# Optimization experiments

Hardware: AMD Instinct MI355X
Metric: run time of the kernel (lower is better)

## Reference

```python
import jax, jax.numpy as jnp
import numpy as np

R_MAX = 5.0          # MACE default cutoff
P_CUT = 6            # polynomial cutoff exponent
AVG_NEIGH = 16.0     # MACE avg_num_neighbors normalization


def _sph_harm(u):
    """Real spherical harmonics l=0..3, e3nn 'component' normalization. u: [E,3] unit vectors -> [E,16]."""
    x, y, z = u[..., 0], u[..., 1], u[..., 2]
    s3, s5, s15 = np.sqrt(3.0), np.sqrt(5.0), np.sqrt(15.0)
    s35_8, s105, s21_8, s7 = np.sqrt(35.0 / 8.0), np.sqrt(105.0), np.sqrt(21.0 / 8.0), np.sqrt(7.0)
    one = jnp.ones_like(x)
    Y = [
        one,
        s3 * x, s3 * y, s3 * z,
        s15 * x * y, s15 * y * z, 0.5 * s5 * (3.0 * z * z - 1.0), s15 * x * z, 0.5 * s15 * (x * x - y * y),
        s35_8 * y * (3.0 * x * x - y * y), s105 * x * y * z, s21_8 * y * (5.0 * z * z - 1.0),
        0.5 * s7 * (5.0 * z * z * z - 3.0 * z), s21_8 * x * (5.0 * z * z - 1.0),
        0.5 * s105 * z * (x * x - y * y), s35_8 * x * (x * x - 3.0 * y * y),
    ]
    return jnp.stack(Y, axis=-1)


def _radial_embedding(r):
    """Bessel basis (8) times polynomial cutoff. r: [E] -> [E,8]."""
    n = jnp.arange(1, 9, dtype=r.dtype)
    rb = np.sqrt(2.0 / R_MAX) * jnp.sin(n * jnp.pi * r[:, None] / R_MAX) / r[:, None]
    uu = jnp.clip(r / R_MAX, 0.0, 1.0)
    p = float(P_CUT)
    f = (1.0 - 0.5 * (p + 1.0) * (p + 2.0) * uu ** p
         + p * (p + 2.0) * uu ** (p + 1.0)
         - 0.5 * p * (p + 1.0) * uu ** (p + 2.0))
    return rb * f[:, None]


def _forward(positions, shifts, node_attrs, W_embed, W_up, W_r1, W_r2, W_lin, W_skip, W_prod, Wcg, Wcg2, edge_index):
    N = positions.shape[0]
    snd, rcv = edge_index[0], edge_index[1]
    vec = positions[rcv] - positions[snd] + shifts            # [E,3]
    r = jnp.sqrt(jnp.maximum(jnp.sum(vec * vec, -1), 1e-12))  # [E]
    u = vec / r[:, None]
    edge_attrs = _sph_harm(u)                                 # [E,16]
    edge_feats = _radial_embedding(r)                         # [E,8]
    L = edge_attrs.shape[-1]
    k = W_embed.shape[1]
    # node embedding: scalars in the l=0 slot
    feats = jnp.zeros((N, k, L), positions.dtype).at[:, :, 0].set(node_attrs @ W_embed)
    invariants = []
    for i in range(W_up.shape[0]):
        up = jnp.einsum('nkL,kc->ncL', feats, W_up[i])                      # linear_up
        Rw = jax.nn.silu(edge_feats @ W_r1[i]) @ W_r2[i]                    # radial MLP [E,k]
        gathered = up[snd] * Rw[:, :, None]                                 # [E,k,16]
        # equivariant tensor product (coupling tensor plays the CG role)
        msg = jnp.einsum('eka,es,ast->ekt', gathered, edge_attrs, Wcg)      # [E,k,16]
        agg = jax.ops.segment_sum(msg, rcv, num_segments=N) / AVG_NEIGH     # scatter-sum
        mid = jnp.einsum('nkL,kc->ncL', agg, W_lin[i])
        # residual skip tensor product with species attrs
        sc = jnp.einsum('nkL,nz,zkc->ncL', feats, node_attrs, W_skip[i])
        # product block: symmetric (quadratic) contraction + linear + skip
        quad = jnp.einsum('nka,nkb,abt->nkt', mid, mid, Wcg2)
        feats = jnp.einsum('nkL,kc->ncL', mid + quad, W_prod[i]) + sc
        invariants.append(feats[:, :, 0])                                   # l=0 invariant slice [N,k]
    return jnp.concatenate(invariants, axis=-1)                             # [N, n_layers*k]


def setup_inputs() -> dict:
    key = jax.random.key(0)
    ks = jax.random.split(key, 12)
    N, E, Z, k, L, NB, H, NL = 8000, 128000, 10, 32, 16, 8, 32, 2
    positions = jax.random.normal(ks[0], (N, 3), dtype=jnp.float32) * 2.0
    edge_index = jax.random.randint(ks[1], (2, E), 0, N, dtype=jnp.int32)
    shifts = jnp.zeros((E, 3), jnp.float32)
    species = jax.random.randint(ks[2], (N,), 0, Z)
    node_attrs = jax.nn.one_hot(species, Z, dtype=jnp.float32)
    W_embed = jax.random.normal(ks[3], (Z, k), dtype=jnp.float32) / np.sqrt(Z)
    W_up = jax.random.normal(ks[4], (NL, k, k), dtype=jnp.float32) / np.sqrt(k)
    W_r1 = jax.random.normal(ks[5], (NL, NB, H), dtype=jnp.float32) / np.sqrt(NB)
    W_r2 = jax.random.normal(ks[6], (NL, H, k), dtype=jnp.float32) / np.sqrt(H)
    W_lin = jax.random.normal(ks[7], (NL, k, k), dtype=jnp.float32) / np.sqrt(k)
    W_skip = jax.random.normal(ks[8], (NL, Z, k, k), dtype=jnp.float32) / np.sqrt(Z * k)
    W_prod = jax.random.normal(ks[9], (NL, k, k), dtype=jnp.float32) / np.sqrt(k)
    Wcg = jax.random.normal(ks[10], (L, L, L), dtype=jnp.float32) * 0.1
    Wcg2 = jax.random.normal(ks[11], (L, L, L), dtype=jnp.float32) * 0.05
    return dict(positions=positions, shifts=shifts, node_attrs=node_attrs, W_embed=W_embed,
                W_up=W_up, W_r1=W_r1, W_r2=W_r2, W_lin=W_lin, W_skip=W_skip, W_prod=W_prod,
                Wcg=Wcg, Wcg2=Wcg2, edge_index=edge_index)


def reference(positions, shifts, node_attrs, W_embed, W_up, W_r1, W_r2, W_lin, W_skip, W_prod, Wcg, Wcg2, edge_index):
    return _forward(positions, shifts, node_attrs, W_embed, W_up, W_r1, W_r2, W_lin, W_skip, W_prod, Wcg, Wcg2, edge_index)
```

## Files before the change

kernel.cpp:

```cpp
#include <hip/hip_runtime.h>
#include <math.h>
#include <stdint.h>

#define N_NODES 8000
#define N_EDGES 128000
#define NZ 10
#define K 32
#define LDIM 16
#define NB 8
#define NH 32
#define NL 2

typedef _Float16 half8 __attribute__((ext_vector_type(8)));
typedef _Float16 half2v __attribute__((ext_vector_type(2)));
typedef __attribute__((ext_vector_type(4))) float f32x4;

#define WAVE_SYNC() do { \
    asm volatile("s_waitcnt lgkmcnt(0)" ::: "memory"); \
    __builtin_amdgcn_wave_barrier(); \
    __builtin_amdgcn_sched_barrier(0); \
} while (0)

#define NBSTRIDE 640

__global__ __launch_bounds__(256) void k_count(const int* __restrict__ ei,
                                               int* __restrict__ counts) {
    int e = blockIdx.x * 256 + threadIdx.x;
    if (e >= N_EDGES) return;
    atomicAdd(&counts[ei[N_EDGES + e]], 1);
}

__global__ __launch_bounds__(1024) void k_scan(const int* __restrict__ counts,
                                               int* __restrict__ row_ptr,
                                               int* __restrict__ woff) {
    __shared__ int s[8192];
    int tid = threadIdx.x;
    for (int j = tid; j < 8192; j += 1024) s[j] = (j < N_NODES) ? counts[j] : 0;
    __syncthreads();
    for (int off = 1; off < 8192; off <<= 1) {
        int v[8];
#pragma unroll
        for (int jj = 0; jj < 8; jj++) {
            int idx = tid + jj*1024;
            v[jj] = s[idx] + ((idx >= off) ? s[idx - off] : 0);
        }
        __syncthreads();
#pragma unroll
        for (int jj = 0; jj < 8; jj++) s[tid + jj*1024] = v[jj];
        __syncthreads();
    }
    for (int j = tid; j <= N_NODES; j += 1024) {
        int v = (j == 0) ? 0 : s[j-1];
        row_ptr[j] = v;
        if (j < N_NODES) woff[j] = v;
    }
}

__global__ __launch_bounds__(256) void k_scatter(const int* __restrict__ ei,
                                                 int* __restrict__ woff,
                                                 int* __restrict__ inv,
                                                 int* __restrict__ snd_csr) {
    int e = blockIdx.x * 256 + threadIdx.x;
    if (e >= N_EDGES) return;
    int r = ei[N_EDGES + e];
    int s = ei[e];
    int pp = atomicAdd(&woff[r], 1);
    inv[e] = pp;
    snd_csr[pp] = s;
}

__global__ __launch_bounds__(256) void k_geom(const float* __restrict__ pos,
                                              const float* __restrict__ shifts,
                                              const int* __restrict__ ei,
                                              const int* __restrict__ inv,
                                              const float* __restrict__ Wcg,
                                              const float* __restrict__ W_r1,
                                              const float* __restrict__ W_r2,
                                              float* __restrict__ Yc,
                                              float* __restrict__ C0c,
                                              float* __restrict__ Rwc0,
                                              float* __restrict__ Rwc1) {
    __shared__ __align__(16) float lW1[2*NB*NH];
    __shared__ __align__(16) float lW2[2*NH*K];
    int tid = threadIdx.x;
    for (int j = tid; j < 2*NB*NH; j += 256) lW1[j] = W_r1[j];
    for (int j = tid; j < 2*NH*K;  j += 256) lW2[j] = W_r2[j];
    __syncthreads();

    int e = blockIdx.x * blockDim.x + tid;
    if (e >= N_EDGES) return;
    int snd = ei[e];
    int rcv = ei[N_EDGES + e];
    int slot = inv[e];
    float vx = pos[rcv*3+0] - pos[snd*3+0] + shifts[e*3+0];
    float vy = pos[rcv*3+1] - pos[snd*3+1] + shifts[e*3+1];
    float vz = pos[rcv*3+2] - pos[snd*3+2] + shifts[e*3+2];
    float r2 = vx*vx + vy*vy + vz*vz;
    float r  = sqrtf(fmaxf(r2, 1e-12f));
    float inv_r = 1.0f / r;
    float x = vx*inv_r, y = vy*inv_r, z = vz*inv_r;

    const float s3    = 1.7320508075688772f;
    const float s5    = 2.2360679774997896f;
    const float s15   = 3.8729833462074170f;
    const float s35_8 = 2.0916500663351885f;
    const float s105  = 10.246950765959598f;
    const float s21_8 = 1.6201851746019651f;
    const float s7    = 2.6457513110645907f;

    float Yv[16];
    Yv[0]  = 1.0f;
    Yv[1]  = s3*x;  Yv[2] = s3*y;  Yv[3] = s3*z;
    Yv[4]  = s15*x*y;
    Yv[5]  = s15*y*z;
    Yv[6]  = 0.5f*s5*(3.0f*z*z - 1.0f);
    Yv[7]  = s15*x*z;
    Yv[8]  = 0.5f*s15*(x*x - y*y);
    Yv[9]  = s35_8*y*(3.0f*x*x - y*y);
    Yv[10] = s105*x*y*z;
    Yv[11] = s21_8*y*(5.0f*z*z - 1.0f);
    Yv[12] = 0.5f*s7*(5.0f*z*z*z - 3.0f*z);
    Yv[13] = s21_8*x*(5.0f*z*z - 1.0f);
    Yv[14] = 0.5f*s105*z*(x*x - y*y);
    Yv[15] = s35_8*x*(x*x - 3.0f*y*y);
#pragma unroll
    for (int j = 0; j < 16; j++) Yc[(size_t)slot*16 + j] = Yv[j];

    {
        float c0[16];
#pragma unroll
        for (int t = 0; t < 16; ++t) c0[t] = 0.0f;
#pragma unroll
        for (int s = 0; s < 16; ++s) {
            const float4* w = (const float4*)(Wcg + s*16);
            float4 w0 = w[0], w1 = w[1], w2 = w[2], w3 = w[3];
            float ys = Yv[s];
            c0[0]+=ys*w0.x;  c0[1]+=ys*w0.y;  c0[2]+=ys*w0.z;  c0[3]+=ys*w0.w;
            c0[4]+=ys*w1.x;  c0[5]+=ys*w1.y;  c0[6]+=ys*w1.z;  c0[7]+=ys*w1.w;
            c0[8]+=ys*w2.x;  c0[9]+=ys*w2.y;  c0[10]+=ys*w2.z; c0[11]+=ys*w2.w;
            c0[12]+=ys*w3.x; c0[13]+=ys*w3.y; c0[14]+=ys*w3.z; c0[15]+=ys*w3.w;
        }
        float* o = C0c + (size_t)slot*16;
#pragma unroll
        for (int tq = 0; tq < 4; ++tq)
            *(float4*)(o + tq*4) = make_float4(c0[tq*4], c0[tq*4+1], c0[tq*4+2], c0[tq*4+3]);
    }

    float uu = fminf(fmaxf(r * 0.2f, 0.0f), 1.0f);
    float u2 = uu*uu;
    float u6 = u2*u2*u2;
    float f  = 1.0f - 28.0f*u6 + 48.0f*u6*uu - 21.0f*u6*u2;
    float c  = 0.632455532033676f * inv_r * f;
    const float PI5 = 3.14159265358979323846f * 0.2f;
    float efr[8];
#pragma unroll
    for (int n = 1; n <= 8; n++) efr[n-1] = c * sinf((float)n * PI5 * r);

#pragma unroll
    for (int L = 0; L < 2; ++L) {
        const float* w1 = lW1 + L*NB*NH;
        const float* w2 = lW2 + L*NH*K;
        float rw[32];
#pragma unroll
        for (int k = 0; k < 32; ++k) rw[k] = 0.0f;
        for (int j = 0; j < NH; ++j) {
            float h = 0.0f;
#pragma unroll
            for (int b = 0; b < NB; ++b) h += efr[b] * w1[b*NH + j];
            float s = h / (1.0f + expf(-h));
            const float4* w2r = (const float4*)(w2 + j*K);
#pragma unroll
            for (int kq = 0; kq < 8; ++kq) {
                float4 w = w2r[kq];
                rw[kq*4+0] += s*w.x; rw[kq*4+1] += s*w.y;
                rw[kq*4+2] += s*w.z; rw[kq*4+3] += s*w.w;
            }
        }
        float* o = (L == 0 ? Rwc0 : Rwc1) + (size_t)slot*32;
#pragma unroll
        for (int kq = 0; kq < 8; ++kq)
            *(float4*)(o + kq*4) = make_float4(rw[kq*4], rw[kq*4+1], rw[kq*4+2], rw[kq*4+3]);
    }
}

__global__ __launch_bounds__(256) void k_ww(const float* __restrict__ We,
                                            const float* __restrict__ Wup0,
                                            float* __restrict__ WW) {
    int i = blockIdx.x * 256 + threadIdx.x;
    if (i >= NZ * K) return;
    int z = i >> 5, c = i & 31;
    float a = 0.0f;
#pragma unroll
    for (int k = 0; k < K; ++k) a += We[z*K + k] * Wup0[k*K + c];
    WW[i] = a;
}

__global__ __launch_bounds__(256) void k_wsym(const float* __restrict__ Wcg2,
                                              float* __restrict__ Wsym) {
    int j = blockIdx.x * 256 + threadIdx.x;
    if (j >= 136*16) return;
    int p = j >> 4, t = j & 15;
    int a = 0;
    for (int aa = 1; aa < 16; ++aa)
        if (p >= aa*16 - (aa*(aa-1))/2) a = aa;
    int b = a + (p - (a*16 - (a*(a-1))/2));
    float v = Wcg2[a*256 + b*16 + t];
    if (b > a) v += Wcg2[b*256 + a*16 + t];
    Wsym[j] = v;
}

__global__ __launch_bounds__(256) void k_embed(const float* __restrict__ attrs,
                                               const float* __restrict__ We,
                                               const float* __restrict__ WW,
                                               float* __restrict__ feats,
                                               float* __restrict__ up0c,
                                               int* __restrict__ spec) {
    int i = blockIdx.x * blockDim.x + threadIdx.x;
    if (i >= N_NODES * K) return;
    int n = i >> 5, k = i & 31;
    float a = 0.0f, b = 0.0f;
#pragma unroll
    for (int z = 0; z < NZ; z++) {
        float av = attrs[n*NZ + z];
        a += av * We[z*K + k];
        b += av * WW[z*K + k];
    }
    float* f = feats + (size_t)n*(K*LDIM) + k*LDIM;
    f[0] = a;
#pragma unroll
    for (int j = 1; j < LDIM; j++) f[j] = 0.0f;
    up0c[(size_t)n*K + k] = b;
    if (k == 0) {
        int sp = 0; float best = -1.0f;
        for (int z = 0; z < NZ; z++) { float v = attrs[n*NZ + z]; if (v > best) { best = v; sp = z; } }
        spec[n] = sp;
    }
}

__device__ __forceinline__ void node_update(float* nb,
                                            const float* lWlin, const float* lWprod,
                                            const float* lWup, const float* lWsym,
                                            const float* __restrict__ Wskip,
                                            float* __restrict__ feats,
                                            const int* __restrict__ spec,
                                            float* __restrict__ out,
                                            int n, int lane, int layer,
                                            _Float16* __restrict__ up_next, int has_up) {
    int c  = lane & 31;
    int th = lane >> 5;
    int to = th * 8;

    float m8[8] = {0,0,0,0,0,0,0,0};
#pragma clang loop unroll_count(4)
    for (int k = 0; k < 32; ++k) {
        float w = lWlin[k*32 + c];
        float4 a0 = *(const float4*)(nb + k*20 + to);
        float4 a1 = *(const float4*)(nb + k*20 + to + 4);
        m8[0]+=a0.x*w; m8[1]+=a0.y*w; m8[2]+=a0.z*w; m8[3]+=a0.w*w;
        m8[4]+=a1.x*w; m8[5]+=a1.y*w; m8[6]+=a1.z*w; m8[7]+=a1.w*w;
    }
    WAVE_SYNC();
    *(float4*)(nb + c*20 + to)     = make_float4(m8[0],m8[1],m8[2],m8[3]);
    *(float4*)(nb + c*20 + to + 4) = make_float4(m8[4],m8[5],m8[6],m8[7]);
    WAVE_SYNC();
    float m[16];
#pragma unroll
    for (int j = 0; j < 4; ++j) {
        float4 v = *(const float4*)(nb + c*20 + j*4);
        m[j*4]=v.x; m[j*4+1]=v.y; m[j*4+2]=v.z; m[j*4+3]=v.w;
    }

    float q8[8] = {0,0,0,0,0,0,0,0};
    {
        int p = 0;
#pragma clang loop unroll(disable)
        for (int a = 0; a < 16; ++a) {
            float ma = m[a];
#pragma clang loop unroll_count(2)
            for (int b = a; b < 16; ++b) {
                float pm = ma * m[b];
                float4 w0 = *(const float4*)(lWsym + p*16 + to);
                float4 w1 = *(const float4*)(lWsym + p*16 + to + 4);
                q8[0]+=pm*w0.x; q8[1]+=pm*w0.y; q8[2]+=pm*w0.z; q8[3]+=pm*w0.w;
                q8[4]+=pm*w1.x; q8[5]+=pm*w1.y; q8[6]+=pm*w1.z; q8[7]+=pm*w1.w;
                ++p;
            }
        }
    }

    WAVE_SYNC();
    *(float4*)(nb + c*20 + to)     = make_float4(m[to]+q8[0],   m[to+1]+q8[1],
                                                 m[to+2]+q8[2], m[to+3]+q8[3]);
    *(float4*)(nb + c*20 + to + 4) = make_float4(m[to+4]+q8[4], m[to+5]+q8[5],
                                                 m[to+6]+q8[6], m[to+7]+q8[7]);
    WAVE_SYNC();

    int sp = spec[n];
    const float* wsk = Wskip + (size_t)sp*1024;
    float* fg = feats + (size_t)n*512;
    float acc8[8] = {0,0,0,0,0,0,0,0};
#pragma clang loop unroll_count(4)
    for (int k = 0; k < 32; ++k) {
        float wp = lWprod[k*32 + c];
        float wv = wsk[k*32 + c];
        float4 s0 = *(const float4*)(nb + k*20 + to);
        float4 s1 = *(const float4*)(nb + k*20 + to + 4);
        float4 f0 = *(const float4*)(fg + k*16 + to);
        float4 f1 = *(const float4*)(fg + k*16 + to + 4);
        acc8[0]+=s0.x*wp+f0.x*wv; acc8[1]+=s0.y*wp+f0.y*wv;
        acc8[2]+=s0.z*wp+f0.z*wv; acc8[3]+=s0.w*wp+f0.w*wv;
        acc8[4]+=s1.x*wp+f1.x*wv; acc8[5]+=s1.y*wp+f1.y*wv;
        acc8[6]+=s1.z*wp+f1.z*wv; acc8[7]+=s1.w*wp+f1.w*wv;
    }
    if (th == 0) out[(size_t)n*(NL*K) + layer*K + c] = acc8[0];
    *(float4*)(fg + c*16 + to)     = make_float4(acc8[0],acc8[1],acc8[2],acc8[3]);
    *(float4*)(fg + c*16 + to + 4) = make_float4(acc8[4],acc8[5],acc8[6],acc8[7]);

    if (has_up) {
        WAVE_SYNC();
        *(float4*)(nb + c*20 + to)     = make_float4(acc8[0],acc8[1],acc8[2],acc8[3]);
        *(float4*)(nb + c*20 + to + 4) = make_float4(acc8[4],acc8[5],acc8[6],acc8[7]);
        WAVE_SYNC();
        float u8[8] = {0,0,0,0,0,0,0,0};
#pragma clang loop unroll_count(4)
        for (int k = 0; k < 32; ++k) {
            float w = lWup[k*32 + c];
            float4 f0 = *(const float4*)(nb + k*20 + to);
            float4 f1 = *(const float4*)(nb + k*20 + to + 4);
            u8[0]+=f0.x*w; u8[1]+=f0.y*w; u8[2]+=f0.z*w; u8[3]+=f0.w*w;
            u8[4]+=f1.x*w; u8[5]+=f1.y*w; u8[6]+=f1.z*w; u8[7]+=f1.w*w;
        }
        half8 h;
#pragma unroll
        for (int j = 0; j < 8; ++j) h[j] = (_Float16)u8[j];
        *(half8*)(up_next + (size_t)n*512 + c*16 + to) = h;
    }
}

__global__ __launch_bounds__(256, 4) void k_fused0(const float* __restrict__ up0c,
                                                   const float* __restrict__ C0c,
                                                   const float* __restrict__ Rwc,
                                                   const int* __restrict__ snd_csr,
                                                   const int* __restrict__ row_ptr,
                                                   const float* __restrict__ Wlin,
                                                   const float* __restrict__ Wskip,
                                                   const float* __restrict__ Wprod,
                                                   const float* __restrict__ WsymG,
                                                   const float* __restrict__ Wup_next,
                                                   float* __restrict__ feats,
                                                   const int* __restrict__ spec,
                                                   float* __restrict__ out,
                                                   _Float16* __restrict__ up_next) {
    __shared__ __align__(16) float lWlin[1024];
    __shared__ __align__(16) float lWprod[1024];
    __shared__ __align__(16) float lWup[1024];
    __shared__ __align__(16) float lWsym[2176];
    __shared__ __align__(16) float buf[4*NBSTRIDE];

    int tid = threadIdx.x;
    for (int j = tid; j < 1024; j += 256) { lWlin[j] = Wlin[j]; lWprod[j] = Wprod[j]; lWup[j] = Wup_next[j]; }
    for (int j = tid; j < 2176; j += 256) lWsym[j] = WsymG[j];
    __syncthreads();

    int wave = tid >> 6, lane = tid & 63;
    int n = blockIdx.x * 4 + wave;
    int k0 = lane & 15, tq = lane >> 4;
    float* nb = buf + wave*NBSTRIDE;

    int start = row_ptr[n], end = row_ptr[n+1];
    float4 acc0 = {0,0,0,0}, acc1 = {0,0,0,0};

    if (start < end) {
        int snd = snd_csr[start];
        float4 c0v = *(const float4*)(C0c + (size_t)start*16 + tq*4);
        float rw0 = Rwc[(size_t)start*32 + k0];
        float rw1 = Rwc[(size_t)start*32 + 16 + k0];
        float u0 = up0c[(size_t)snd*32 + k0];
        float u1 = up0c[(size_t)snd*32 + 16 + k0];

        for (int ii = start; ii < end; ++ii) {
            int ip = (ii + 1 < end) ? ii + 1 : ii;
            int nsnd = snd_csr[ip];
            float4 nc0v = *(const float4*)(C0c + (size_t)ip*16 + tq*4);
            float nrw0 = Rwc[(size_t)ip*32 + k0];
            float nrw1 = Rwc[(size_t)ip*32 + 16 + k0];
            float nu0 = up0c[(size_t)nsnd*32 + k0];
            float nu1 = up0c[(size_t)nsnd*32 + 16 + k0];

            float g0 = rw0 * u0, g1 = rw1 * u1;
            acc0.x += g0*c0v.x; acc0.y += g0*c0v.y; acc0.z += g0*c0v.z; acc0.w += g0*c0v.w;
            acc1.x += g1*c0v.x; acc1.y += g1*c0v.y; acc1.z += g1*c0v.z; acc1.w += g1*c0v.w;

            c0v = nc0v; rw0 = nrw0; rw1 = nrw1; u0 = nu0; u1 = nu1;
        }
    }

    *(float4*)(nb + k0*20 + tq*4)      = make_float4(acc0.x*0.0625f, acc0.y*0.0625f,
                                                     acc0.z*0.0625f, acc0.w*0.0625f);
    *(float4*)(nb + (16+k0)*20 + tq*4) = make_float4(acc1.x*0.0625f, acc1.y*0.0625f,
                                                     acc1.z*0.0625f, acc1.w*0.0625f);
    WAVE_SYNC();

    node_update(nb, lWlin, lWprod, lWup, lWsym, Wskip, feats, spec, out, n, lane, 0, up_next, 1);
}

__global__ __launch_bounds__(256, 3) void k_fused1(const _Float16* __restrict__ up,
                                                   const float* __restrict__ Yc,
                                                   const float* __restrict__ Rwc,
                                                   const int* __restrict__ snd_csr,
                                                   const int* __restrict__ row_ptr,
                                                   const float* __restrict__ Wcg,
                                                   const float* __restrict__ Wlin,
                                                   const float* __restrict__ Wskip,
                                                   const float* __restrict__ Wprod,
                                                   const float* __restrict__ WsymG,
                                                   float* __restrict__ feats,
                                                   const int* __restrict__ spec,
                                                   float* __restrict__ out) {
    __shared__ __align__(16) float lWlin[1024];
    __shared__ __align__(16) float lWprod[1024];
    __shared__ __align__(16) float lWsym[2176];
    __shared__ __align__(16) float buf[4*NBSTRIDE];

    int tid = threadIdx.x;
    for (int j = tid; j < 1024; j += 256) { lWlin[j] = Wlin[j]; lWprod[j] = Wprod[j]; }
    for (int j = tid; j < 2176; j += 256) lWsym[j] = WsymG[j];
    __syncthreads();

    int wave = tid >> 6, lane = tid & 63;
    int n = blockIdx.x * 4 + wave;
    int t0 = lane & 15;
    int g  = lane >> 4;
    int h  = g & 1;
    int eo = g >> 1;
    float* nb = buf + wave*NBSTRIDE;

    half2v wrh[16][4];
#pragma unroll
    for (int s = 0; s < 16; ++s)
#pragma unroll
        for (int q = 0; q < 4; ++q) {
            half2v w;
            w[0] = (_Float16)Wcg[(8*h + 2*q    )*256 + s*16 + t0];
            w[1] = (_Float16)Wcg[(8*h + 2*q + 1)*256 + s*16 + t0];
            wrh[s][q] = w;
        }

    int start = row_ptr[n], end = row_ptr[n+1];
    f32x4 accL = {0.f,0.f,0.f,0.f}, accH = {0.f,0.f,0.f,0.f};

    if (start < end) {
        int i0 = start + eo;     bool v0 = i0 < end; int q0 = v0 ? i0 : start;
        int i1 = i0 + 2;         bool v1 = i1 < end; int q1 = v1 ? i1 : start;
        int i2 = i0 + 4;         bool v2 = i2 < end; int q2 = v2 ? i2 : start;
        int snd0 = snd_csr[q0], snd1 = snd_csr[q1];
        int snd2 = snd_csr[q2];

        const float4* Y4 = (const float4*)(Yc + (size_t)q0*16);
        float4 y0=Y4[0], y1=Y4[1], y2=Y4[2], y3=Y4[3];
        float rwL = v0 ? Rwc[(size_t)q0*32 + t0]      : 0.0f;
        float rwH = v0 ? Rwc[(size_t)q0*32 + 16 + t0] : 0.0f;
        half8 u0L = *(const half8*)(up + (size_t)snd0*512 + t0*16 + 8*h);
        half8 u0H = *(const half8*)(up + (size_t)snd0*512 + (16+t0)*16 + 8*h);
        half8 u1L = *(const half8*)(up + (size_t)snd1*512 + t0*16 + 8*h);
        half8 u1H = *(const half8*)(up + (size_t)snd1*512 + (16+t0)*16 + 8*h);

        int npair = (end - start + 1) >> 1;
        for (int p = 0; p < npair; ++p) {
            half8 u2L = *(const half8*)(up + (size_t)snd2*512 + t0*16 + 8*h);
            half8 u2H = *(const half8*)(up + (size_t)snd2*512 + (16+t0)*16 + 8*h);
            int in1 = start + 2*(p+1) + eo; bool vn1 = in1 < end; int qn1 = vn1 ? in1 : start;
            const float4* nY = (const float4*)(Yc + (size_t)qn1*16);
            float4 ny0=nY[0], ny1=nY[1], ny2=nY[2], ny3=nY[3];
            float nrwL = vn1 ? Rwc[(size_t)qn1*32 + t0]      : 0.0f;
            float nrwH = vn1 ? Rwc[(size_t)qn1*32 + 16 + t0] : 0.0f;
            int in3 = start + 2*(p+3) + eo; bool vn3 = in3 < end; int qn3 = vn3 ? in3 : start;
            int snd3 = snd_csr[qn3];

            float yv[16] = {y0.x,y0.y,y0.z,y0.w, y1.x,y1.y,y1.z,y1.w,
                            y2.x,y2.y,y2.z,y2.w, y3.x,y3.y,y3.z,y3.w};
            half2v ch[4];
#pragma unroll
            for (int q = 0; q < 4; ++q) { half2v z; z[0]=(_Float16)0.f; z[1]=(_Float16)0.f; ch[q]=z; }
#pragma unroll
            for (int s = 0; s < 16; ++s) {
                _Float16 yh = (_Float16)yv[s];
                half2v yb; yb[0] = yh; yb[1] = yh;
#pragma unroll
                for (int q = 0; q < 4; ++q) ch[q] += yb * wrh[s][q];
            }
            half8 bf;
#pragma unroll
            for (int q = 0; q < 4; ++q) { bf[2*q] = ch[q][0]; bf[2*q+1] = ch[q][1]; }

            half8 rvL, rvH;
            _Float16 rwLh = (_Float16)rwL, rwHh = (_Float16)rwH;
#pragma unroll
            for (int j = 0; j < 8; ++j) { rvL[j] = rwLh; rvH[j] = rwHh; }
            half8 afL = u0L * rvL;
            half8 afH = u0H * rvH;

            accL = __builtin_amdgcn_mfma_f32_16x16x32_f16(afL, bf, accL, 0, 0, 0);
            accH = __builtin_amdgcn_mfma_f32_16x16x32_f16(afH, bf, accH, 0, 0, 0);

            y0=ny0; y1=ny1; y2=ny2; y3=ny3;
            rwL=nrwL; rwH=nrwH;
            u0L=u1L; u0H=u1H; u1L=u2L; u1H=u2H;
            snd2 = snd3;
        }
    }

#pragma unroll
    for (int e = 0; e < 4; ++e) {
        nb[(4*g + e)*20 + t0]      = accL[e] * 0.0625f;
        nb[(16 + 4*g + e)*20 + t0] = accH[e] * 0.0625f;
    }
    WAVE_SYNC();

    node_update(nb, lWlin, lWprod, (const float*)nullptr, lWsym, Wskip, feats, spec, out,
                n, lane, 1, (_Float16*)nullptr, 0);
}

extern "C" void kernel_launch(void* const* d_in, const int* in_sizes, int n_in,
                              void* d_out, int out_size, void* d_ws, size_t ws_size,
                              hipStream_t stream) {
    const float* pos     = (const float*)d_in[0];
    const float* shifts  = (const float*)d_in[1];
    const float* attrs   = (const float*)d_in[2];
    const float* W_embed = (const float*)d_in[3];
    const float* W_up    = (const float*)d_in[4];
    const float* W_r1    = (const float*)d_in[5];
    const float* W_r2    = (const float*)d_in[6];
    const float* W_lin   = (const float*)d_in[7];
    const float* W_skip  = (const float*)d_in[8];
    const float* W_prod  = (const float*)d_in[9];
    const float* Wcg     = (const float*)d_in[10];
    const float* Wcg2    = (const float*)d_in[11];
    const int*   ei      = (const int*)d_in[12];
    float* out = (float*)d_out;

    uint8_t* p = (uint8_t*)d_ws;
    auto alloc = [&](size_t bytes) -> void* {
        void* r = (void*)p;
        p += (bytes + 255) & ~size_t(255);
        return r;
    };
    float* Yc        = (float*)alloc((size_t)N_EDGES * 16 * sizeof(float));
    float* C0c       = (float*)alloc((size_t)N_EDGES * 16 * sizeof(float));
    float* Rwc0      = (float*)alloc((size_t)N_EDGES * K  * sizeof(float));
    float* Rwc1      = (float*)alloc((size_t)N_EDGES * K  * sizeof(float));
    float* feats     = (float*)alloc((size_t)N_NODES * K * LDIM * sizeof(float));
    _Float16* up_h   = (_Float16*)alloc((size_t)N_NODES * K * LDIM * sizeof(_Float16));
    float* up0c      = (float*)alloc((size_t)N_NODES * K * sizeof(float));
    float* WW        = (float*)alloc((size_t)NZ * K * sizeof(float));
    float* Wsym      = (float*)alloc((size_t)136 * 16 * sizeof(float));
    int* counts   = (int*)alloc((size_t)N_NODES * sizeof(int));
    int* woff     = (int*)alloc((size_t)N_NODES * sizeof(int));
    int* row_ptr  = (int*)alloc((size_t)(N_NODES + 1) * sizeof(int));
    int* inv      = (int*)alloc((size_t)N_EDGES * sizeof(int));
    int* snd_csr  = (int*)alloc((size_t)N_EDGES * sizeof(int));
    int* spec     = (int*)alloc((size_t)N_NODES * sizeof(int));

    hipMemsetAsync(counts, 0, N_NODES * sizeof(int), stream);
    k_count<<<(N_EDGES + 255) / 256, 256, 0, stream>>>(ei, counts);
    k_scan<<<1, 1024, 0, stream>>>(counts, row_ptr, woff);
    k_scatter<<<(N_EDGES + 255) / 256, 256, 0, stream>>>(ei, woff, inv, snd_csr);
    k_geom<<<(N_EDGES + 255) / 256, 256, 0, stream>>>(pos, shifts, ei, inv, Wcg,
                                                      W_r1, W_r2, Yc, C0c, Rwc0, Rwc1);
    k_ww<<<2, 256, 0, stream>>>(W_embed, W_up, WW);
    k_wsym<<<(136*16 + 255) / 256, 256, 0, stream>>>(Wcg2, Wsym);
    k_embed<<<(N_NODES * K + 255) / 256, 256, 0, stream>>>(attrs, W_embed, WW, feats, up0c, spec);

    k_fused0<<<N_NODES/4, 256, 0, stream>>>(up0c, C0c, Rwc0, snd_csr, row_ptr,
                                            W_lin, W_skip, W_prod, Wsym,
                                            W_up + (size_t)1*K*K,
                                            feats, spec, out, up_h);

    k_fused1<<<N_NODES/4, 256, 0, stream>>>(up_h, Yc, Rwc1, snd_csr, row_ptr, Wcg,
                                            W_lin + (size_t)1*K*K,
                                            W_skip + (size_t)1*NZ*K*K,
                                            W_prod + (size_t)1*K*K, Wsym,
                                            feats, spec, out);
}
```

Before: 225.3 us.

## Sort nodes by degree buckets so waves in a block have similar work

Adds a counting sort of nodes by in-degree (histogram, scan, scatter) that produces a node permutation. Both fused per-node kernels read their node index through this map, so the four waves in a block handle nodes of similar degree. This aims to cut the idle time of waves that finish early and wait on the slowest wave in the block. It adds three small kernels and a memset, and it loses the locality of consecutive node ids, which can hurt cache reuse of feature writes and CSR reads.

```diff
diff --git a/kernel.cpp b/kernel.cpp
--- a/kernel.cpp
+++ b/kernel.cpp
@@ -10,6 +10,7 @@
 #define NB 8
 #define NH 32
 #define NL 2
+#define DBUCKETS 64
 
 typedef _Float16 half8 __attribute__((ext_vector_type(8)));
 typedef _Float16 half2v __attribute__((ext_vector_type(2)));
@@ -67,6 +68,30 @@
     int pp = atomicAdd(&woff[r], 1);
     inv[e] = pp;
     snd_csr[pp] = s;
+}
+
+__global__ __launch_bounds__(256) void k_dhist(const int* __restrict__ counts,
+                                               int* __restrict__ dcount) {
+    int n = blockIdx.x * 256 + threadIdx.x;
+    if (n >= N_NODES) return;
+    int d = counts[n]; if (d > DBUCKETS-1) d = DBUCKETS-1;
+    atomicAdd(&dcount[d], 1);
+}
+__global__ __launch_bounds__(64) void k_dscan(const int* __restrict__ dcount,
+                                              int* __restrict__ doff) {
+    if (threadIdx.x == 0) {
+        int acc = 0;
+        for (int i = 0; i < DBUCKETS; ++i) { doff[i] = acc; acc += dcount[i]; }
+    }
+}
+__global__ __launch_bounds__(256) void k_dscatter(const int* __restrict__ counts,
+                                                  int* __restrict__ doff,
+                                                  int* __restrict__ nmap) {
+    int n = blockIdx.x * 256 + threadIdx.x;
+    if (n >= N_NODES) return;
+    int d = counts[n]; if (d > DBUCKETS-1) d = DBUCKETS-1;
+    int pos = atomicAdd(&doff[d], 1);
+    nmap[pos] = n;
 }
 
 __global__ __launch_bounds__(256) void k_geom(const float* __restrict__ pos,
@@ -342,6 +367,7 @@
                                                    const float* __restrict__ Rwc,
                                                    const int* __restrict__ snd_csr,
                                                    const int* __restrict__ row_ptr,
+                                                   const int* __restrict__ nmap,
                                                    const float* __restrict__ Wlin,
                                                    const float* __restrict__ Wskip,
                                                    const float* __restrict__ Wprod,
@@ -363,7 +389,7 @@
     __syncthreads();
 
     int wave = tid >> 6, lane = tid & 63;
-    int n = blockIdx.x * 4 + wave;
+    int n = nmap[blockIdx.x * 4 + wave];
     int k0 = lane & 15, tq = lane >> 4;
     float* nb = buf + wave*NBSTRIDE;
 
@@ -409,6 +435,7 @@
                                                    const float* __restrict__ Rwc,
                                                    const int* __restrict__ snd_csr,
                                                    const int* __restrict__ row_ptr,
+                                                   const int* __restrict__ nmap,
                                                    const float* __restrict__ Wcg,
                                                    const float* __restrict__ Wlin,
                                                    const float* __restrict__ Wskip,
@@ -428,7 +455,7 @@
     __syncthreads();
 
     int wave = tid >> 6, lane = tid & 63;
-    int n = blockIdx.x * 4 + wave;
+    int n = nmap[blockIdx.x * 4 + wave];
     int t0 = lane & 15;
     int g  = lane >> 4;
     int h  = g & 1;
@@ -560,23 +587,31 @@
     int* inv      = (int*)alloc((size_t)N_EDGES * sizeof(int));
     int* snd_csr  = (int*)alloc((size_t)N_EDGES * sizeof(int));
     int* spec     = (int*)alloc((size_t)N_NODES * sizeof(int));
+    int* dcount   = (int*)alloc((size_t)DBUCKETS * sizeof(int));
+    int* doff     = (int*)alloc((size_t)DBUCKETS * sizeof(int));
+    int* nmap     = (int*)alloc((size_t)N_NODES * sizeof(int));
 
     hipMemsetAsync(counts, 0, N_NODES * sizeof(int), stream);
+    hipMemsetAsync(dcount, 0, DBUCKETS * sizeof(int), stream);
     k_count<<<(N_EDGES + 255) / 256, 256, 0, stream>>>(ei, counts);
     k_scan<<<1, 1024, 0, stream>>>(counts, row_ptr, woff);
     k_scatter<<<(N_EDGES + 255) / 256, 256, 0, stream>>>(ei, woff, inv, snd_csr);
+    k_dhist<<<(N_NODES + 255) / 256, 256, 0, stream>>>(counts, dcount);
+    k_dscan<<<1, 64, 0, stream>>>(dcount, doff);
+    k_dscatter<<<(N_NODES + 255) / 256, 256, 0, stream>>>(counts, doff, nmap);
+
     k_geom<<<(N_EDGES + 255) / 256, 256, 0, stream>>>(pos, shifts, ei, inv, Wcg,
                                                       W_r1, W_r2, Yc, C0c, Rwc0, Rwc1);
     k_ww<<<2, 256, 0, stream>>>(W_embed, W_up, WW);
     k_wsym<<<(136*16 + 255) / 256, 256, 0, stream>>>(Wcg2, Wsym);
     k_embed<<<(N_NODES * K + 255) / 256, 256, 0, stream>>>(attrs, W_embed, WW, feats, up0c, spec);
 
-    k_fused0<<<N_NODES/4, 256, 0, stream>>>(up0c, C0c, Rwc0, snd_csr, row_ptr,
+    k_fused0<<<N_NODES/4, 256, 0, stream>>>(up0c, C0c, Rwc0, snd_csr, row_ptr, nmap,
                                             W_lin, W_skip, W_prod, Wsym,
                                             W_up + (size_t)1*K*K,
                                             feats, spec, out, up_h);
 
-    k_fused1<<<N_NODES/4, 256, 0, stream>>>(up_h, Yc, Rwc1, snd_csr, row_ptr, Wcg,
+    k_fused1<<<N_NODES/4, 256, 0, stream>>>(up_h, Yc, Rwc1, snd_csr, row_ptr, nmap, Wcg,
                                             W_lin + (size_t)1*K*K,
                                             W_skip + (size_t)1*NZ*K*K,
                                             W_prod + (size_t)1*K*K, Wsym,
```

Result: slower. 276.5 us (+22.7%).
